# Kernel optimization log

Measured on AMD Instinct MI355X. Metric: run time of the kernel, lower is better.

The kernel has to match this reference:

```python
import jax, jax.numpy as jnp
import numpy as np

B, N, D, H = 16, 1024, 768, 12
HD = D // H
SCALE = HD ** -0.5


def setup_inputs() -> dict:
    key = jax.random.key(0)
    ks = jax.random.split(key, 7)
    s = D ** -0.5  # keep activations well-scaled
    return {
        "x": jax.random.normal(ks[0], (B, N, D), dtype=jnp.float32),
        "Wq": jax.random.normal(ks[1], (D, D), dtype=jnp.float32) * s,
        "bq": jax.random.normal(ks[2], (D,), dtype=jnp.float32) * 0.01,
        "Wk": jax.random.normal(ks[3], (D, D), dtype=jnp.float32) * s,
        "bk": jax.random.normal(ks[4], (D,), dtype=jnp.float32) * 0.01,
        "Wp": jax.random.normal(ks[5], (D, D), dtype=jnp.float32) * s,
        "bp": jax.random.normal(ks[6], (D,), dtype=jnp.float32) * 0.01,
    }


def reference(x, Wq, bq, Wk, bk, Wp, bp):
    # Faithful to source: V uses the K projection (bug in original, Vm unused).
    q = x @ Wq.T + bq  # [B,N,D]
    k = x @ Wk.T + bk
    v = k              # V = Km(x) in the original code
    # split heads -> [B,H,N,HD]
    q = q.reshape(B, N, H, HD).transpose(0, 2, 1, 3)
    k = k.reshape(B, N, H, HD).transpose(0, 2, 1, 3)
    v = v.reshape(B, N, H, HD).transpose(0, 2, 1, 3)
    scores = jnp.einsum("bhqd,bhkd->bhqk", q, k) * SCALE  # [B,H,N,N]
    attn = jax.nn.softmax(scores, axis=-1)
    out = jnp.einsum("bhqk,bhkd->bhqd", attn, v)  # [B,H,N,HD]
    out = out.transpose(0, 2, 1, 3).reshape(B, N, D)
    return out @ Wp.T + bp
```

## Files before the change

kernel.cpp:

```cpp
#include <hip/hip_runtime.h>
#include <hip/hip_bf16.h>


#define DEV static __device__ __forceinline__

typedef __attribute__((ext_vector_type(8)))  short  short8;
typedef __attribute__((ext_vector_type(4)))  short  short4v;
typedef __attribute__((ext_vector_type(4)))  float  f32x4;
typedef __attribute__((ext_vector_type(16))) float  f32x16;
typedef __attribute__((ext_vector_type(4)))  unsigned short ushort4v;
typedef __attribute__((ext_vector_type(8)))  unsigned short ushort8v;
typedef __attribute__((ext_vector_type(4)))  unsigned int   u32x4;

#define QSCALE 0.180336880f

DEV unsigned short f2bf(float x) {
  unsigned int u = __float_as_uint(x);
  u = u + 0x7fffu + ((u >> 16) & 1u);
  return (unsigned short)(u >> 16);
}

DEV float exp2v(float x) {
  float r;
  asm("v_exp_f32 %0, %1" : "=v"(r) : "v"(x));
  return r;
}

DEV unsigned cvtpk(float a, float b) {
  unsigned r;
  asm("v_cvt_pk_bf16_f32 %0, %1, %2" : "=v"(r) : "v"(a), "v"(b));
  return r;
}

#define GLOAD_LDS16(g, l)                                                     \
  __builtin_amdgcn_global_load_lds(                                           \
      (const __attribute__((address_space(1))) void*)(g),                     \
      (__attribute__((address_space(3))) void*)(l), 16, 0, 0)

__global__ __launch_bounds__(256) void k_prep(const float* __restrict__ x,
                                              const float* __restrict__ Wq,
                                              const float* __restrict__ Wk,
                                              const float* __restrict__ Wp,
                                              const float* __restrict__ bq,
                                              const float* __restrict__ bk,
                                              unsigned short* __restrict__ xb,
                                              unsigned short* __restrict__ wqb,
                                              unsigned short* __restrict__ wkb,
                                              unsigned short* __restrict__ wpb,
                                              float* __restrict__ bqk) {
  int blk = blockIdx.x;
  if (blk < 1728) {
    const float* src = (blk < 576) ? Wq : (blk < 1152) ? Wk : Wp;
    unsigned short* dst = (blk < 576) ? wqb : (blk < 1152) ? wkb : wpb;
    int i = (blk % 576) * 256 + threadIdx.x;
    f32x4 v = *(const f32x4*)(src + (size_t)i * 4);
    ushort4v o;
    o[0] = f2bf(v[0]); o[1] = f2bf(v[1]); o[2] = f2bf(v[2]); o[3] = f2bf(v[3]);
    *(ushort4v*)(dst + (size_t)i * 4) = o;
  } else if (blk < 1734) {
    int i = (blk - 1728) * 256 + threadIdx.x;
    if (i < 768) bqk[i] = bq[i];
    else if (i < 1536) bqk[i] = bk[i - 768];
  } else {
    size_t i = (size_t)(blk - 1734) * 256 + threadIdx.x;
    const f32x4* src = (const f32x4*)(x + i * 8);
    f32x4 a = src[0], b4 = src[1];
    ushort8v o;
    o[0] = f2bf(a[0]);  o[1] = f2bf(a[1]);  o[2] = f2bf(a[2]);  o[3] = f2bf(a[3]);
    o[4] = f2bf(b4[0]); o[5] = f2bf(b4[1]); o[6] = f2bf(b4[2]); o[7] = f2bf(b4[3]);
    *(ushort8v*)(xb + i * 8) = o;
  }
}

template <int MODE>
__global__ __launch_bounds__(256) void k_gemm_bt(const unsigned short* __restrict__ A,
                                                 const unsigned short* __restrict__ W,
                                                 const float* __restrict__ bias,
                                                 void* __restrict__ Cv,
                                                 unsigned short* __restrict__ kT2g,
                                                 int M, int N, int K) {
  __shared__ char lds[32768];
  char* ldsA = lds;
  char* ldsB = lds + 16384;
  const int tid  = threadIdx.x;
  const int wid  = tid >> 6;
  const int lane = tid & 63;
  const int row0 = blockIdx.x * 128;
  const int col0 = blockIdx.y * 128;
  const int wr = (wid >> 1) * 64;
  const int wc = (wid & 1) * 64;
  const int lr = lane & 15;
  const int lg = lane >> 4;

  f32x4 acc[4][4];
#pragma unroll
  for (int m = 0; m < 4; ++m)
#pragma unroll
    for (int n = 0; n < 4; ++n)
#pragma unroll
      for (int r = 0; r < 4; ++r) acc[m][n][r] = 0.f;

  for (int kt = 0; kt < K; kt += 64) {
    __syncthreads();
#pragma unroll
    for (int p = 0; p < 4; ++p) {
      int c = p * 256 + tid;
      int r  = c >> 3;
      int cb = ((c & 7) << 4) ^ ((r & 7) << 4);
      const char* ga = (const char*)(A + (size_t)(row0 + r) * K + kt) + cb;
      GLOAD_LDS16(ga, ldsA + c * 16);
      const char* gb = (const char*)(W + (size_t)(col0 + r) * K + kt) + cb;
      GLOAD_LDS16(gb, ldsB + c * 16);
    }
    asm volatile("s_waitcnt vmcnt(0)" ::: "memory");
    __syncthreads();
#pragma unroll
    for (int kk = 0; kk < 2; ++kk) {
      short8 af[4], bf[4];
#pragma unroll
      for (int m = 0; m < 4; ++m) {
        int row = wr + m * 16 + lr;
        int a   = row * 128 + ((kk * 64 + lg * 16) ^ ((row & 7) << 4));
        af[m] = *(const short8*)(ldsA + a);
        int col = wc + m * 16 + lr;
        int b   = col * 128 + ((kk * 64 + lg * 16) ^ ((col & 7) << 4));
        bf[m] = *(const short8*)(ldsB + b);
      }
#pragma unroll
      for (int m = 0; m < 4; ++m)
#pragma unroll
        for (int n = 0; n < 4; ++n)
          acc[m][n] = __builtin_amdgcn_mfma_f32_16x16x32_bf16(af[m], bf[n], acc[m][n], 0, 0, 0);
    }
  }

  const int r0g = row0 + wr + lg * 4;
  const int c0g = col0 + wc + lr;
  float bv[4];
#pragma unroll
  for (int n = 0; n < 4; ++n) bv[n] = bias[c0g + n * 16];

  if constexpr (MODE == 2) {
    const bool kh = (col0 >= 768);
    unsigned short* dst = (unsigned short*)Cv + (kh ? ((size_t)16384 * 768 - 768) : 0);
    const float sc = kh ? 1.0f : QSCALE;
#pragma unroll
    for (int m = 0; m < 4; ++m)
#pragma unroll
      for (int n = 0; n < 4; ++n) {
        ushort4v t4;
#pragma unroll
        for (int r = 0; r < 4; ++r) {
          float v = (acc[m][n][r] + bv[n]) * sc;
          unsigned short bfv = f2bf(v);
          dst[(size_t)(r0g + m * 16 + r) * 768 + (c0g + n * 16)] = bfv;
          t4[r] = bfv;
        }
        if (kh) {
          int hd2  = c0g + n * 16 - 768;
          int rowb = r0g + m * 16;
          int b_ = rowb >> 10, nn = rowb & 1023;
          size_t kbase = ((((size_t)(b_ * 12 + (hd2 >> 6)) * 32 + (nn >> 5)) * 64
                           + (hd2 & 63)) * 32 + (nn & 31));
          *(ushort4v*)(kT2g + kbase) = t4;
        }
      }
  } else {
#pragma unroll
    for (int m = 0; m < 4; ++m)
#pragma unroll
      for (int n = 0; n < 4; ++n)
#pragma unroll
        for (int r = 0; r < 4; ++r) {
          float v = acc[m][n][r] + bv[n];
          ((float*)Cv)[(size_t)(r0g + m * 16 + r) * N + (c0g + n * 16)] = v;
        }
  }
}

__global__ __launch_bounds__(256) void k_attn(const unsigned short* __restrict__ qg,
                                              const unsigned short* __restrict__ kg,
                                              const unsigned short* __restrict__ kT2,
                                              unsigned short* __restrict__ og) {
  __shared__ char lds[32768];
  const int tid  = threadIdx.x;
  const int w    = tid >> 6;
  const int lane = tid & 63;
  const int q32  = lane & 31;
  const int hi   = lane >> 5;
  const int blk  = (blockIdx.x & 7) * 192 + (blockIdx.x >> 3);
  const int qc   = blk & 7;
  const int bh   = blk >> 3;
  const int h = bh % 12, b = bh / 12;
  const int qbase = qc * 128 + w * 32;

  const unsigned short* Qp = qg + (size_t)(b * 1024 + qbase + q32) * 768 + h * 64;
  short8 qf[4];
#pragma unroll
  for (int c = 0; c < 4; ++c) qf[c] = *(const short8*)(Qp + c * 16 + hi * 8);

  short8 ones;
#pragma unroll
  for (int j = 0; j < 8; ++j) ones[j] = (short)0x3F80;

  const int sr = tid >> 3, sp = tid & 7;
  const unsigned short* ksrc = kg + (size_t)(b * 1024 + sr) * 768 + h * 64 + ((sp ^ (sr & 7)) << 3);
  const int vh = tid >> 2, vp = tid & 3;
  const unsigned short* vsrc = kT2 + (size_t)bh * 65536 + (size_t)vh * 32 + ((vp ^ ((vh >> 1) & 3)) << 3);

  f32x16 o0, o1, lacc, zro;
#pragma unroll
  for (int r = 0; r < 16; ++r) { o0[r] = 0.f; o1[r] = 0.f; lacc[r] = 0.f; zro[r] = 0.f; }

  GLOAD_LDS16(ksrc,          lds + tid * 16);
  GLOAD_LDS16(ksrc + 24576,  lds + 4096 + tid * 16);
  GLOAD_LDS16(vsrc,          lds + 8192 + tid * 16);
  GLOAD_LDS16(vsrc + 2048,   lds + 12288 + tid * 16);

  const int kfo0 = q32 * 128;
  const int vswz = (q32 >> 1) & 3;

  for (int t = 0; t < 16; ++t) {
    const int bo = (t & 1) << 14;
    asm volatile("s_waitcnt vmcnt(0)" ::: "memory");
    __syncthreads();
    if (t + 1 < 16) {
      const int bn = bo ^ 16384;
      const unsigned short* kn = ksrc + (size_t)(t + 1) * 49152;
      const unsigned short* vn = vsrc + (size_t)(t + 1) * 4096;
      GLOAD_LDS16(kn,         lds + bn + tid * 16);
      GLOAD_LDS16(kn + 24576, lds + bn + 4096 + tid * 16);
      GLOAD_LDS16(vn,         lds + bn + 8192 + tid * 16);
      GLOAD_LDS16(vn + 2048,  lds + bn + 12288 + tid * 16);
    }

#pragma unroll
    for (int st = 0; st < 2; ++st) {
      const int kb0 = bo + st * 4096 + kfo0;
      const int vb0 = bo + 8192 + st * 4096;

      short8 kf0 = *(const short8*)(lds + kb0 + ((hi ^ (q32 & 7)) << 4));
      f32x16 s = __builtin_amdgcn_mfma_f32_32x32x16_bf16(kf0, qf[0], zro, 0, 0, 0);
#pragma unroll
      for (int c = 1; c < 4; ++c) {
        short8 kf = *(const short8*)(lds + kb0 + (((c * 2 + hi) ^ (q32 & 7)) << 4));
        s = __builtin_amdgcn_mfma_f32_32x32x16_bf16(kf, qf[c], s, 0, 0, 0);
      }

      short8 vf[2][2];
#pragma unroll
      for (int f = 0; f < 2; ++f)
#pragma unroll
        for (int s2 = 0; s2 < 2; ++s2)
          vf[s2][f] = *(const short8*)(lds + vb0 + (f * 32 + q32) * 64 +
                                       (((s2 * 2 + hi) ^ vswz) << 4));

      float p[16];
#pragma unroll
      for (int r = 0; r < 16; ++r) p[r] = exp2v(s[r]);

      unsigned pw[8];
#pragma unroll
      for (int i = 0; i < 8; ++i) pw[i] = cvtpk(p[2 * i], p[2 * i + 1]);

      {
        unsigned x0 = pw[0], y0 = pw[2], x1 = pw[1], y1 = pw[3];
        asm("v_permlane32_swap_b32 %0, %1" : "+v"(x0), "+v"(y0));
        asm("v_permlane32_swap_b32 %0, %1" : "+v"(x1), "+v"(y1));
        union { u32x4 wv; short8 sv; } u;
        u.wv[0] = x0; u.wv[1] = x1; u.wv[2] = y0; u.wv[3] = y1;
        o0   = __builtin_amdgcn_mfma_f32_32x32x16_bf16(vf[0][0], u.sv, o0, 0, 0, 0);
        o1   = __builtin_amdgcn_mfma_f32_32x32x16_bf16(vf[0][1], u.sv, o1, 0, 0, 0);
        lacc = __builtin_amdgcn_mfma_f32_32x32x16_bf16(ones,     u.sv, lacc, 0, 0, 0);
      }
      {
        unsigned x0 = pw[4], y0 = pw[6], x1 = pw[5], y1 = pw[7];
        asm("v_permlane32_swap_b32 %0, %1" : "+v"(x0), "+v"(y0));
        asm("v_permlane32_swap_b32 %0, %1" : "+v"(x1), "+v"(y1));
        union { u32x4 wv; short8 sv; } u;
        u.wv[0] = x0; u.wv[1] = x1; u.wv[2] = y0; u.wv[3] = y1;
        o0   = __builtin_amdgcn_mfma_f32_32x32x16_bf16(vf[1][0], u.sv, o0, 0, 0, 0);
        o1   = __builtin_amdgcn_mfma_f32_32x32x16_bf16(vf[1][1], u.sv, o1, 0, 0, 0);
        lacc = __builtin_amdgcn_mfma_f32_32x32x16_bf16(ones,     u.sv, lacc, 0, 0, 0);
      }
    }
  }

  __syncthreads();
  float inv = 1.f / lacc[0];
  char* lw = lds + w * 4608;
#pragma unroll
  for (int mg = 0; mg < 4; ++mg) {
    short4v t;
#pragma unroll
    for (int i = 0; i < 4; ++i) t[i] = (short)f2bf(o0[mg * 4 + i] * inv);
    *(short4v*)(lw + q32 * 144 + mg * 16 + hi * 8) = t;
#pragma unroll
    for (int i = 0; i < 4; ++i) t[i] = (short)f2bf(o1[mg * 4 + i] * inv);
    *(short4v*)(lw + q32 * 144 + 64 + mg * 16 + hi * 8) = t;
  }
  __syncthreads();
  const size_t obase = (size_t)(b * 1024 + qbase) * 768 + h * 64;
#pragma unroll
  for (int pp = 0; pp < 4; ++pp) {
    int chunk = pp * 64 + lane;
    int qr = chunk >> 3, cc = chunk & 7;
    short8 v = *(const short8*)(lw + qr * 144 + cc * 16);
    *(short8*)(og + obase + (size_t)qr * 768 + cc * 8) = v;
  }
}

extern "C" void kernel_launch(void* const* d_in, const int* in_sizes, int n_in,
                              void* d_out, int out_size, void* d_ws, size_t ws_size,
                              hipStream_t stream) {
  const float* x  = (const float*)d_in[0];
  const float* Wq = (const float*)d_in[1];
  const float* bq = (const float*)d_in[2];
  const float* Wk = (const float*)d_in[3];
  const float* bk = (const float*)d_in[4];
  const float* Wp = (const float*)d_in[5];
  const float* bp = (const float*)d_in[6];
  float* out = (float*)d_out;
  char* ws = (char*)d_ws;

  const size_t XB = (size_t)16384 * 768 * 2;
  const size_t WB = (size_t)768 * 768 * 2;
  if (ws_size < 3 * XB + 3 * WB + 6144) return;

  unsigned short* xb  = (unsigned short*)(ws);
  unsigned short* qb  = (unsigned short*)(ws + XB);
  unsigned short* kb  = (unsigned short*)(ws + 2 * XB);
  unsigned short* wqb = (unsigned short*)(ws + 3 * XB);
  unsigned short* wkb = (unsigned short*)(ws + 3 * XB + WB);
  unsigned short* wpb = (unsigned short*)(ws + 3 * XB + 2 * WB);
  float*          bqk = (float*)(ws + 3 * XB + 3 * WB);
  unsigned short* ab  = xb;
  unsigned short* kTb = (unsigned short*)d_out;

  k_prep<<<7878, 256, 0, stream>>>(x, Wq, Wk, Wp, bq, bk, xb, wqb, wkb, wpb, bqk);

  k_gemm_bt<2><<<dim3(128, 12), 256, 0, stream>>>(xb, wqb, bqk, qb, kTb, 16384, 1536, 768);
  k_attn<<<1536, 256, 0, stream>>>(qb, kb, kTb, ab);
  k_gemm_bt<0><<<dim3(128, 6), 256, 0, stream>>>(ab, wpb, bp, out, nullptr, 16384, 768, 768);
}
```

Baseline: 161.7 us.

## Process two 32-row query blocks per wave in attention to reuse K/V tiles

Each wave now handles 64 queries (two 32-row sub-blocks) instead of 32, so each workgroup covers 256 queries and the grid halves to 768 blocks. K and V fragments loaded from LDS are reused across both query sub-blocks, which halves global K/V traffic per query and LDS reads per MFMA. The cost is twice the accumulator registers, which may lower occupancy, and fewer blocks (768 over 256 CUs) giving coarser load balance.

```diff
diff --git a/kernel.cpp b/kernel.cpp
--- a/kernel.cpp
+++ b/kernel.cpp
@@ -188,16 +188,19 @@
   const int lane = tid & 63;
   const int q32  = lane & 31;
   const int hi   = lane >> 5;
-  const int blk  = (blockIdx.x & 7) * 192 + (blockIdx.x >> 3);
-  const int qc   = blk & 7;
-  const int bh   = blk >> 3;
+  const int blk  = (blockIdx.x & 7) * 96 + (blockIdx.x >> 3);
+  const int qc   = blk & 3;
+  const int bh   = blk >> 2;
   const int h = bh % 12, b = bh / 12;
-  const int qbase = qc * 128 + w * 32;
+  const int qbase = qc * 256 + w * 64;
 
   const unsigned short* Qp = qg + (size_t)(b * 1024 + qbase + q32) * 768 + h * 64;
-  short8 qf[4];
-#pragma unroll
-  for (int c = 0; c < 4; ++c) qf[c] = *(const short8*)(Qp + c * 16 + hi * 8);
+  short8 qf[2][4];
+#pragma unroll
+  for (int qb = 0; qb < 2; ++qb)
+#pragma unroll
+    for (int c = 0; c < 4; ++c)
+      qf[qb][c] = *(const short8*)(Qp + (size_t)qb * 32 * 768 + c * 16 + hi * 8);
 
   short8 ones;
 #pragma unroll
@@ -208,9 +211,13 @@
   const int vh = tid >> 2, vp = tid & 3;
   const unsigned short* vsrc = kT2 + (size_t)bh * 65536 + (size_t)vh * 32 + ((vp ^ ((vh >> 1) & 3)) << 3);
 
-  f32x16 o0, o1, lacc, zro;
-#pragma unroll
-  for (int r = 0; r < 16; ++r) { o0[r] = 0.f; o1[r] = 0.f; lacc[r] = 0.f; zro[r] = 0.f; }
+  f32x16 o0[2], o1[2], lacc[2], zro;
+#pragma unroll
+  for (int r = 0; r < 16; ++r) {
+    o0[0][r] = 0.f; o1[0][r] = 0.f; lacc[0][r] = 0.f;
+    o0[1][r] = 0.f; o1[1][r] = 0.f; lacc[1][r] = 0.f;
+    zro[r] = 0.f;
+  }
 
   GLOAD_LDS16(ksrc,          lds + tid * 16);
   GLOAD_LDS16(ksrc + 24576,  lds + 4096 + tid * 16);
@@ -239,13 +246,10 @@
       const int kb0 = bo + st * 4096 + kfo0;
       const int vb0 = bo + 8192 + st * 4096;
 
-      short8 kf0 = *(const short8*)(lds + kb0 + ((hi ^ (q32 & 7)) << 4));
-      f32x16 s = __builtin_amdgcn_mfma_f32_32x32x16_bf16(kf0, qf[0], zro, 0, 0, 0);
-#pragma unroll
-      for (int c = 1; c < 4; ++c) {
-        short8 kf = *(const short8*)(lds + kb0 + (((c * 2 + hi) ^ (q32 & 7)) << 4));
-        s = __builtin_amdgcn_mfma_f32_32x32x16_bf16(kf, qf[c], s, 0, 0, 0);
-      }
+      short8 kf[4];
+#pragma unroll
+      for (int c = 0; c < 4; ++c)
+        kf[c] = *(const short8*)(lds + kb0 + (((c * 2 + hi) ^ (q32 & 7)) << 4));
 
       short8 vf[2][2];
 #pragma unroll
@@ -255,58 +259,70 @@
           vf[s2][f] = *(const short8*)(lds + vb0 + (f * 32 + q32) * 64 +
                                        (((s2 * 2 + hi) ^ vswz) << 4));
 
-      float p[16];
-#pragma unroll
-      for (int r = 0; r < 16; ++r) p[r] = exp2v(s[r]);
-
-      unsigned pw[8];
-#pragma unroll
-      for (int i = 0; i < 8; ++i) pw[i] = cvtpk(p[2 * i], p[2 * i + 1]);
-
-      {
-        unsigned x0 = pw[0], y0 = pw[2], x1 = pw[1], y1 = pw[3];
-        asm("v_permlane32_swap_b32 %0, %1" : "+v"(x0), "+v"(y0));
-        asm("v_permlane32_swap_b32 %0, %1" : "+v"(x1), "+v"(y1));
-        union { u32x4 wv; short8 sv; } u;
-        u.wv[0] = x0; u.wv[1] = x1; u.wv[2] = y0; u.wv[3] = y1;
-        o0   = __builtin_amdgcn_mfma_f32_32x32x16_bf16(vf[0][0], u.sv, o0, 0, 0, 0);
-        o1   = __builtin_amdgcn_mfma_f32_32x32x16_bf16(vf[0][1], u.sv, o1, 0, 0, 0);
-        lacc = __builtin_amdgcn_mfma_f32_32x32x16_bf16(ones,     u.sv, lacc, 0, 0, 0);
+#pragma unroll
+      for (int qb = 0; qb < 2; ++qb) {
+        f32x16 s = __builtin_amdgcn_mfma_f32_32x32x16_bf16(kf[0], qf[qb][0], zro, 0, 0, 0);
+#pragma unroll
+        for (int c = 1; c < 4; ++c)
+          s = __builtin_amdgcn_mfma_f32_32x32x16_bf16(kf[c], qf[qb][c], s, 0, 0, 0);
+
+        float p[16];
+#pragma unroll
+        for (int r = 0; r < 16; ++r) p[r] = exp2v(s[r]);
+
+        unsigned pw[8];
+#pragma unroll
+        for (int i = 0; i < 8; ++i) pw[i] = cvtpk(p[2 * i], p[2 * i + 1]);
+
+        {
+          unsigned x0 = pw[0], y0 = pw[2], x1 = pw[1], y1 = pw[3];
+          asm("v_permlane32_swap_b32 %0, %1" : "+v"(x0), "+v"(y0));
+          asm("v_permlane32_swap_b32 %0, %1" : "+v"(x1), "+v"(y1));
+          union { u32x4 wv; short8 sv; } u;
+          u.wv[0] = x0; u.wv[1] = x1; u.wv[2] = y0; u.wv[3] = y1;
+          o0[qb]   = __builtin_amdgcn_mfma_f32_32x32x16_bf16(vf[0][0], u.sv, o0[qb], 0, 0, 0);
+          o1[qb]   = __builtin_amdgcn_mfma_f32_32x32x16_bf16(vf[0][1], u.sv, o1[qb], 0, 0, 0);
+          lacc[qb] = __builtin_amdgcn_mfma_f32_32x32x16_bf16(ones,     u.sv, lacc[qb], 0, 0, 0);
+        }
+        {
+          unsigned x0 = pw[4], y0 = pw[6], x1 = pw[5], y1 = pw[7];
+          asm("v_permlane32_swap_b32 %0, %1" : "+v"(x0), "+v"(y0));
+          asm("v_permlane32_swap_b32 %0, %1" : "+v"(x1), "+v"(y1));
+          union { u32x4 wv; short8 sv; } u;
+          u.wv[0] = x0; u.wv[1] = x1; u.wv[2] = y0; u.wv[3] = y1;
+          o0[qb]   = __builtin_amdgcn_mfma_f32_32x32x16_bf16(vf[1][0], u.sv, o0[qb], 0, 0, 0);
+          o1[qb]   = __builtin_amdgcn_mfma_f32_32x32x16_bf16(vf[1][1], u.sv, o1[qb], 0, 0, 0);
+          lacc[qb] = __builtin_amdgcn_mfma_f32_32x32x16_bf16(ones,     u.sv, lacc[qb], 0, 0, 0);
+        }
       }
-      {
-        unsigned x0 = pw[4], y0 = pw[6], x1 = pw[5], y1 = pw[7];
-        asm("v_permlane32_swap_b32 %0, %1" : "+v"(x0), "+v"(y0));
-        asm("v_permlane32_swap_b32 %0, %1" : "+v"(x1), "+v"(y1));
-        union { u32x4 wv; short8 sv; } u;
-        u.wv[0] = x0; u.wv[1] = x1; u.wv[2] = y0; u.wv[3] = y1;
-        o0   = __builtin_amdgcn_mfma_f32_32x32x16_bf16(vf[1][0], u.sv, o0, 0, 0, 0);
-        o1   = __builtin_amdgcn_mfma_f32_32x32x16_bf16(vf[1][1], u.sv, o1, 0, 0, 0);
-        lacc = __builtin_amdgcn_mfma_f32_32x32x16_bf16(ones,     u.sv, lacc, 0, 0, 0);
-      }
     }
   }
 
   __syncthreads();
-  float inv = 1.f / lacc[0];
   char* lw = lds + w * 4608;
 #pragma unroll
-  for (int mg = 0; mg < 4; ++mg) {
-    short4v t;
-#pragma unroll
-    for (int i = 0; i < 4; ++i) t[i] = (short)f2bf(o0[mg * 4 + i] * inv);
-    *(short4v*)(lw + q32 * 144 + mg * 16 + hi * 8) = t;
-#pragma unroll
-    for (int i = 0; i < 4; ++i) t[i] = (short)f2bf(o1[mg * 4 + i] * inv);
-    *(short4v*)(lw + q32 * 144 + 64 + mg * 16 + hi * 8) = t;
-  }
-  __syncthreads();
-  const size_t obase = (size_t)(b * 1024 + qbase) * 768 + h * 64;
-#pragma unroll
-  for (int pp = 0; pp < 4; ++pp) {
-    int chunk = pp * 64 + lane;
-    int qr = chunk >> 3, cc = chunk & 7;
-    short8 v = *(const short8*)(lw + qr * 144 + cc * 16);
-    *(short8*)(og + obase + (size_t)qr * 768 + cc * 8) = v;
+  for (int qb = 0; qb < 2; ++qb) {
+    float inv = 1.f / lacc[qb][0];
+#pragma unroll
+    for (int mg = 0; mg < 4; ++mg) {
+      short4v t;
+#pragma unroll
+      for (int i = 0; i < 4; ++i) t[i] = (short)f2bf(o0[qb][mg * 4 + i] * inv);
+      *(short4v*)(lw + q32 * 144 + mg * 16 + hi * 8) = t;
+#pragma unroll
+      for (int i = 0; i < 4; ++i) t[i] = (short)f2bf(o1[qb][mg * 4 + i] * inv);
+      *(short4v*)(lw + q32 * 144 + 64 + mg * 16 + hi * 8) = t;
+    }
+    __syncthreads();
+    const size_t obase = (size_t)(b * 1024 + qbase + qb * 32) * 768 + h * 64;
+#pragma unroll
+    for (int pp = 0; pp < 4; ++pp) {
+      int chunk = pp * 64 + lane;
+      int qr = chunk >> 3, cc = chunk & 7;
+      short8 v = *(const short8*)(lw + qr * 144 + cc * 16);
+      *(short8*)(og + obase + (size_t)qr * 768 + cc * 8) = v;
+    }
+    __syncthreads();
   }
 }
 
@@ -340,6 +356,6 @@
   k_prep<<<7878, 256, 0, stream>>>(x, Wq, Wk, Wp, bq, bk, xb, wqb, wkb, wpb, bqk);
 
   k_gemm_bt<2><<<dim3(128, 12), 256, 0, stream>>>(xb, wqb, bqk, qb, kTb, 16384, 1536, 768);
-  k_attn<<<1536, 256, 0, stream>>>(qb, kb, kTb, ab);
+  k_attn<<<768, 256, 0, stream>>>(qb, kb, kTb, ab);
   k_gemm_bt<0><<<dim3(128, 6), 256, 0, stream>>>(ab, wpb, bp, out, nullptr, 16384, 768, 768);
 }
```

Measured after the change: 162.7 us. No clear change (+0.6%).
